# Kernel optimization log

Hardware: AMD Instinct MI355X
Metric: run time of the kernel (lower is better)

Reference implementation:

```python
import jax, jax.numpy as jnp
import numpy as np

ALPHA = 0.05  # steady-state adaptive alpha (current_step >= warmup_steps)
EPS = 1e-8    # torch cosine_similarity norm clamp

N = 8192
D = 512


def setup_inputs() -> dict:
    key = jax.random.key(0)
    k1, k2 = jax.random.split(key)
    old_emb = jax.random.normal(k1, (N, D), dtype=jnp.float32)
    new_emb = jax.random.normal(k2, (N, D), dtype=jnp.float32)
    return {"old_emb": old_emb, "new_emb": new_emb}


def _featurewise_ot(hidden_old, hidden_new, alpha):
    # nearest-neighbor match by cosine similarity (k=1 topk == argmax)
    old_n = hidden_old / jnp.maximum(jnp.linalg.norm(hidden_old, axis=1, keepdims=True), EPS)
    new_n = hidden_new / jnp.maximum(jnp.linalg.norm(hidden_new, axis=1, keepdims=True), EPS)
    sim = old_n @ new_n.T                      # [n1, n2]
    idx = jnp.argmax(sim, axis=1)              # [n1]
    expanded = hidden_new[idx]                 # [n1, d]

    # batched per-column sort-based OT alignment (replaces the python loop over d)
    h_src = jnp.sort(hidden_old, axis=0)                       # sorted old, per column
    order = jnp.argsort(expanded, axis=0)                      # idx_tgt per column
    h_tgt = jnp.take_along_axis(expanded, order, axis=0)       # sorted target, per column
    delta = alpha * (h_src - h_tgt)                            # [n1, d]
    cols = jnp.broadcast_to(jnp.arange(expanded.shape[1]), order.shape)
    update = jnp.zeros_like(expanded).at[order, cols].set(delta)  # inverse-permutation scatter
    return expanded + update


def reference(old_emb, new_emb):
    aligned_old = _featurewise_ot(old_emb, new_emb, ALPHA)
    return (1.0 - ALPHA) * new_emb + ALPHA * aligned_old
```

## Files before the change

kernel.cpp:

```cpp
#include <hip/hip_runtime.h>
#include <hip/hip_bf16.h>
#include <stdint.h>

#define NROWS 8192
#define DIM 512
#define MARGIN 0.03f
#define OVF_CAP 32

typedef unsigned long long u64;
typedef uint32_t u32;
using bf16x8 = __attribute__((ext_vector_type(8))) short;
using ushort8 = __attribute__((ext_vector_type(8))) unsigned short;
using f32x4 = __attribute__((ext_vector_type(4))) float;

__device__ __forceinline__ u32 f2o(float f){
  u32 u = __float_as_uint(f);
  return (u & 0x80000000u) ? ~u : (u | 0x80000000u);
}
__device__ __forceinline__ float o2f(u32 o){
  u32 u = (o & 0x80000000u) ? (o & 0x7FFFFFFFu) : ~o;
  return __uint_as_float(u);
}
__device__ __forceinline__ unsigned short bfbits(float f){
  __hip_bfloat16 h = __float2bfloat16(f);
  return *reinterpret_cast<unsigned short*>(&h);
}
__device__ __forceinline__ unsigned short f2o16(unsigned short b){
  return (b & 0x8000u) ? (unsigned short)~b : (unsigned short)(b | 0x8000u);
}
__device__ __forceinline__ float b16f(unsigned short b){
  u32 u = (u32)b << 16;
  return __uint_as_float(u);
}
typedef __attribute__((address_space(1))) const void gvoid;
typedef __attribute__((address_space(3))) void svoid;
__device__ __forceinline__ void gll16(const void* g, void* l){
  __builtin_amdgcn_global_load_lds((gvoid*)g, (svoid*)l, 16, 0, 0);
}

__device__ __forceinline__ int HIDX(int b){ return b + (b >> 5); }

__global__ void kconvnorm(const float* __restrict__ olde, const float* __restrict__ newe,
                          unsigned short* __restrict__ abf, unsigned short* __restrict__ bbf,
                          float* __restrict__ invn, u32* __restrict__ cnt){
  int row = blockIdx.x * 4 + (threadIdx.x >> 6);
  int lane = threadIdx.x & 63;
  if (blockIdx.x < 32) cnt[blockIdx.x * 256 + threadIdx.x] = 0u;
  bool isnew = row >= NROWS;
  int r = isnew ? row - NROWS : row;
  const float* src = (isnew ? newe : olde) + (size_t)r * DIM + lane * 8;
  unsigned short* dst = (isnew ? bbf : abf) + (size_t)r * DIM + lane * 8;
  float4 v0 = *(const float4*)src, v1 = *(const float4*)(src + 4);
  ushort8 wv = { bfbits(v0.x), bfbits(v0.y), bfbits(v0.z), bfbits(v0.w),
                 bfbits(v1.x), bfbits(v1.y), bfbits(v1.z), bfbits(v1.w) };
  *(ushort8*)dst = wv;
  if (isnew){
    float s = v0.x*v0.x + v0.y*v0.y + v0.z*v0.z + v0.w*v0.w
            + v1.x*v1.x + v1.y*v1.y + v1.z*v1.z + v1.w*v1.w;
    #pragma unroll
    for (int off = 32; off > 0; off >>= 1) s += __shfl_down(s, off);
    if (lane == 0) invn[r] = 1.0f / fmaxf(sqrtf(s), 1e-8f);
  }
}

__global__ void knorm(const float* __restrict__ x, float* __restrict__ invn,
                      u32* __restrict__ cnt){
  int row = blockIdx.x * 4 + (threadIdx.x >> 6);
  int lane = threadIdx.x & 63;
  if (threadIdx.x < 4) cnt[blockIdx.x * 4 + threadIdx.x] = 0u;
  const float4* xr = (const float4*)(x + (size_t)row * DIM);
  float s = 0.f;
  #pragma unroll
  for (int k = 0; k < 2; ++k){
    float4 v = xr[lane + 64 * k];
    s += v.x * v.x + v.y * v.y + v.z * v.z + v.w * v.w;
  }
  #pragma unroll
  for (int off = 32; off > 0; off >>= 1) s += __shfl_down(s, off);
  if (lane == 0) invn[row] = 1.0f / fmaxf(sqrtf(s), 1e-8f);
}

__device__ __forceinline__ void argmax_epilogue(
    f32x4 (&acc)[2][8], const float* __restrict__ invn,
    int m0, int n0w, int ntile, int wr, int c16, int g,
    u64* __restrict__ Tt, u64* __restrict__ ovf, u32* __restrict__ cnt){
  float invc[8];
  #pragma unroll
  for (int nj = 0; nj < 8; ++nj) invc[nj] = invn[n0w + nj * 16 + c16];
  #pragma unroll
  for (int mi = 0; mi < 2; ++mi){
    #pragma unroll
    for (int reg = 0; reg < 4; ++reg){
      float bv = -3.4e38f; int bj = 0;
      #pragma unroll
      for (int nj = 0; nj < 8; ++nj){
        float v = acc[mi][nj][reg] * invc[nj];
        if (v > bv){ bv = v; bj = nj; }
      }
      int gj = n0w + bj * 16 + c16;
      u64 pk = ((u64)f2o(bv) << 32) | (u32)(~(u32)gj);
      #pragma unroll
      for (int m = 1; m < 16; m <<= 1){
        u64 o = __shfl_xor(pk, m);
        pk = pk > o ? pk : o;
      }
      int grow = m0 + wr * 32 + mi * 16 + g * 4 + reg;
      if (c16 == 0) Tt[(size_t)grow * 64 + ntile] = pk;
      float thr = o2f((u32)(pk >> 32)) - MARGIN;
      int tj = (int)~((u32)pk);
      #pragma unroll
      for (int nj = 0; nj < 8; ++nj){
        float v = acc[mi][nj][reg] * invc[nj];
        int j = n0w + nj * 16 + c16;
        if (v >= thr && j != tj){
          u32 pos = atomicAdd(&cnt[grow], 1u);
          if (pos < OVF_CAP) ovf[(size_t)grow * OVF_CAP + pos] = ((u64)f2o(v) << 32) | (u32)j;
        }
      }
    }
  }
}

__global__ __launch_bounds__(512) void kgemm2(
    const unsigned short* __restrict__ Abf, const unsigned short* __restrict__ Bbf,
    const float* __restrict__ invn, u64* __restrict__ Tt,
    u64* __restrict__ ovf, u32* __restrict__ cnt){
  __shared__ unsigned short As[2][128 * 32];
  __shared__ unsigned short Bs[2][256 * 32];
  const int t = threadIdx.x;
  const int lane = t & 63, w = t >> 6;
  const int c16 = lane & 15, g = lane >> 4;
  const int wr = w >> 1, wc = w & 1;
  int bid = blockIdx.x;
  int xcd = bid & 7, s = bid >> 3;
  int bm = (xcd & 1) * 32 + (s >> 3);
  int bn = (xcd >> 1) * 8 + (s & 7);
  const int m0 = bm * 128, n0 = bn * 256;

  f32x4 acc[2][8];
  #pragma unroll
  for (int mi = 0; mi < 2; ++mi)
    #pragma unroll
    for (int nj = 0; nj < 8; ++nj) acc[mi][nj] = {0.f, 0.f, 0.f, 0.f};

  const int srow = t >> 2;
  const int part = t & 3;
  const int scq = (part ^ ((srow >> 1) & 3)) * 8;
  const int scq2 = (part ^ (((srow + 128) >> 1) & 3)) * 8;

  auto stage = [&](int b, int k0){
    gll16(Abf + (size_t)(m0 + srow) * DIM + k0 + scq, (void*)&As[b][(w * 16) * 32]);
    gll16(Bbf + (size_t)(n0 + srow) * DIM + k0 + scq, (void*)&Bs[b][(w * 16) * 32]);
    gll16(Bbf + (size_t)(n0 + srow + 128) * DIM + k0 + scq2, (void*)&Bs[b][(128 + w * 16) * 32]);
  };

  auto compute = [&](int b){
    bf16x8 af[2], bfr[8];
    #pragma unroll
    for (int mi = 0; mi < 2; ++mi){
      int ra = wr * 32 + mi * 16 + c16;
      af[mi] = *(const bf16x8*)&As[b][ra * 32 + (g ^ ((ra >> 1) & 3)) * 8];
    }
    #pragma unroll
    for (int nj = 0; nj < 8; ++nj){
      int rb = wc * 128 + nj * 16 + c16;
      bfr[nj] = *(const bf16x8*)&Bs[b][rb * 32 + (g ^ ((rb >> 1) & 3)) * 8];
    }
    #pragma unroll
    for (int mi = 0; mi < 2; ++mi)
      #pragma unroll
      for (int nj = 0; nj < 8; ++nj)
        acc[mi][nj] = __builtin_amdgcn_mfma_f32_16x16x32_bf16(af[mi], bfr[nj], acc[mi][nj], 0, 0, 0);
  };

  stage(0, 0);
  stage(1, 32);
  #pragma unroll 1
  for (int kt = 0; kt < 15; ++kt){
    asm volatile("s_waitcnt vmcnt(3)" ::: "memory");
    __builtin_amdgcn_s_barrier();
    compute(kt & 1);
    __builtin_amdgcn_s_barrier();
    if (kt < 14) stage(kt & 1, (kt + 2) * 32);
  }
  asm volatile("s_waitcnt vmcnt(0)" ::: "memory");
  __builtin_amdgcn_s_barrier();
  compute(1);

  argmax_epilogue(acc, invn, m0, n0 + wc * 128, bn * 2 + wc, wr, c16, g, Tt, ovf, cnt);
}

__global__ __launch_bounds__(256) void kgemm_fb(
    const float* __restrict__ A, const float* __restrict__ B,
    const float* __restrict__ invn, u64* __restrict__ Tt,
    u64* __restrict__ ovf, u32* __restrict__ cnt){
  __shared__ short As[128 * 40];
  __shared__ short Bs[128 * 40];
  const int t = threadIdx.x;
  const int lane = t & 63, w = t >> 6;
  const int c16 = lane & 15, g = lane >> 4;
  const int m0 = blockIdx.y * 128, n0 = blockIdx.x * 128;

  f32x4 acc[2][8];
  #pragma unroll
  for (int mi = 0; mi < 2; ++mi)
    #pragma unroll
    for (int nj = 0; nj < 8; ++nj) acc[mi][nj] = {0.f, 0.f, 0.f, 0.f};

  for (int k0 = 0; k0 < DIM; k0 += 32){
    #pragma unroll
    for (int it = 0; it < 2; ++it){
      int s = t + it * 256;
      int row = s >> 2, part = s & 3;
      const float4* ga = (const float4*)(A + (size_t)(m0 + row) * DIM + k0 + part * 8);
      float4 a0 = ga[0], a1 = ga[1];
      bf16x8 ha = { (short)bfbits(a0.x), (short)bfbits(a0.y), (short)bfbits(a0.z), (short)bfbits(a0.w),
                    (short)bfbits(a1.x), (short)bfbits(a1.y), (short)bfbits(a1.z), (short)bfbits(a1.w) };
      *(bf16x8*)(&As[row * 40 + part * 8]) = ha;
      const float4* gb = (const float4*)(B + (size_t)(n0 + row) * DIM + k0 + part * 8);
      float4 b0 = gb[0], b1 = gb[1];
      bf16x8 hb = { (short)bfbits(b0.x), (short)bfbits(b0.y), (short)bfbits(b0.z), (short)bfbits(b0.w),
                    (short)bfbits(b1.x), (short)bfbits(b1.y), (short)bfbits(b1.z), (short)bfbits(b1.w) };
      *(bf16x8*)(&Bs[row * 40 + part * 8]) = hb;
    }
    __syncthreads();
    bf16x8 af[2], bfr[8];
    #pragma unroll
    for (int mi = 0; mi < 2; ++mi)
      af[mi] = *(const bf16x8*)(&As[(w * 32 + mi * 16 + c16) * 40 + g * 8]);
    #pragma unroll
    for (int nj = 0; nj < 8; ++nj)
      bfr[nj] = *(const bf16x8*)(&Bs[(nj * 16 + c16) * 40 + g * 8]);
    #pragma unroll
    for (int mi = 0; mi < 2; ++mi)
      #pragma unroll
      for (int nj = 0; nj < 8; ++nj)
        acc[mi][nj] = __builtin_amdgcn_mfma_f32_16x16x32_bf16(af[mi], bfr[nj], acc[mi][nj], 0, 0, 0);
    __syncthreads();
  }
  argmax_epilogue(acc, invn, m0, n0, blockIdx.x, w, c16, g, Tt, ovf, cnt);
}

__global__ __launch_bounds__(256) void kresolve(
    const float* __restrict__ A, const float* __restrict__ B,
    const float* __restrict__ invn, const u64* __restrict__ Tt,
    const u64* __restrict__ ovf, const u32* __restrict__ cnt,
    int* __restrict__ idx){
  const int r = blockIdx.x * 4 + (threadIdx.x >> 6);
  const int lane = threadIdx.x & 63;
  u64 e = Tt[(size_t)r * 64 + lane];
  u64 m = e;
  #pragma unroll
  for (int s = 1; s < 64; s <<= 1){ u64 o = __shfl_xor(m, s); m = m > o ? m : o; }
  float W = o2f((u32)(m >> 32)) - MARGIN;
  bool inw = o2f((u32)(e >> 32)) >= W;
  u64 bal = __ballot(inw);
  u32 nov_raw = cnt[r];
  int nov = nov_raw > OVF_CAP ? OVF_CAP : (int)nov_raw;
  u64 oe = (lane < nov) ? ovf[(size_t)r * OVF_CAP + lane] : 0ull;
  bool oin = (lane < nov) && (o2f((u32)(oe >> 32)) >= W);
  u64 bal2 = __ballot(oin);
  if (nov_raw <= OVF_CAP && __popcll(bal) == 1 && bal2 == 0ull){
    if (lane == 0) idx[r] = (int)~((u32)m);
    return;
  }
  const float* ar = A + (size_t)r * DIM;
  u64 best = 0ull;
  auto eval = [&](int j){
    const float* br = B + (size_t)j * DIM;
    float s = 0.f;
    for (int k = lane; k < DIM; k += 64) s = fmaf(ar[k], br[k], s);
    #pragma unroll
    for (int o = 32; o > 0; o >>= 1) s += __shfl_xor(s, o);
    s *= invn[j];
    u64 p = ((u64)f2o(s) << 32) | (u32)(~(u32)j);
    best = best > p ? best : p;
  };
  if (nov_raw > OVF_CAP){
    for (int j = 0; j < NROWS; ++j) eval(j);
  } else {
    u64 mm = bal;
    while (mm){
      int b = __ffsll((unsigned long long)mm) - 1;
      int j = (int)~((u32)__shfl(e, b));
      eval(j);
      mm &= mm - 1;
    }
    mm = bal2;
    while (mm){
      int b = __ffsll((unsigned long long)mm) - 1;
      int j = (int)(u32)__shfl(oe, b);
      eval(j);
      mm &= mm - 1;
    }
  }
  if (lane == 0) idx[r] = (int)~((u32)best);
}

__global__ void kexpand(const float* __restrict__ newe, const int* __restrict__ idx,
                        float* __restrict__ expd){
  int i = blockIdx.x * 2 + (threadIdx.x >> 7);
  int c = (threadIdx.x & 127) * 4;
  int j = idx[i];
  *(float4*)(expd + (size_t)i * DIM + c) =
      *(const float4*)(newe + (size_t)j * DIM + c);
}

__global__ __launch_bounds__(256) void ktrans(
    const float* __restrict__ olde, unsigned short* __restrict__ oldT){
  __shared__ unsigned short tile[64][80];
  const int e0 = (blockIdx.x >> 3) * 64;
  const int c0 = (blockIdx.x & 7) * 64;
  const int t = threadIdx.x;
  {
    int r = t >> 2, cp = t & 3;
    const float4* src = (const float4*)(olde + (size_t)(e0 + r) * DIM + c0 + cp * 16);
    #pragma unroll
    for (int q = 0; q < 4; ++q){
      float4 v = src[q];
      int cc = cp * 16 + q * 4;
      tile[cc + 0][r] = bfbits(v.x);
      tile[cc + 1][r] = bfbits(v.y);
      tile[cc + 2][r] = bfbits(v.z);
      tile[cc + 3][r] = bfbits(v.w);
    }
  }
  __syncthreads();
  {
    int cR = t >> 2, ep = t & 3;
    ushort8* dst = (ushort8*)(oldT + (size_t)(c0 + cR) * NROWS + e0 + ep * 16);
    dst[0] = *(ushort8*)&tile[cR][ep * 16];
    dst[1] = *(ushort8*)&tile[cR][ep * 16 + 8];
  }
}

__device__ __forceinline__ void scan8192(u32* hist, u32* wsums, int t, int lane, int w){
  u32 v[8]; u32 ts = 0;
  #pragma unroll
  for (int k = 0; k < 8; ++k){ v[k] = hist[HIDX(t * 8 + k)]; ts += v[k]; }
  u32 inc = ts;
  #pragma unroll
  for (int off = 1; off < 64; off <<= 1){
    u32 o = (u32)__shfl_up((int)inc, off);
    if (lane >= off) inc += o;
  }
  if (lane == 63) wsums[w] = inc;
  __syncthreads();
  u32 wb = 0;
  #pragma unroll
  for (int i = 0; i < 16; ++i){ u32 x = wsums[i]; if (i < w) wb += x; }
  u32 run = wb + inc - ts;
  #pragma unroll
  for (int k = 0; k < 8; ++k){ u32 x = v[k]; hist[HIDX(t * 8 + k)] = run; run += x; }
}

__global__ __launch_bounds__(1024) void ksort4(
    const unsigned short* __restrict__ oldT, const float* __restrict__ newe,
    const int* __restrict__ idx, float* __restrict__ out){
  __shared__ u32 hist[8448];
  __shared__ unsigned short vals[NROWS];
  __shared__ u32 wsums[16];
  const int bid = blockIdx.x;
  const int c = (bid & 7) * 64 + (bid >> 3);
  const int t = threadIdx.x;
  const int lane = t & 63, w = t >> 6;

  #pragma unroll
  for (int k = 0; k < 8; ++k) hist[t + k * 1024] = 0;
  if (t < 256) hist[8192 + t] = 0;
  ushort8 ov = *(const ushort8*)(oldT + (size_t)c * NROWS + t * 8);
  __syncthreads();
  int oc[8];
  #pragma unroll
  for (int k = 0; k < 8; ++k){
    oc[k] = (int)((u32)f2o16((unsigned short)ov[k]) >> 3);
    atomicAdd(&hist[HIDX(oc[k])], 1u);
  }
  __syncthreads();
  scan8192(hist, wsums, t, lane, w);
  __syncthreads();
  #pragma unroll
  for (int k = 0; k < 8; ++k){
    u32 pos = atomicAdd(&hist[HIDX(oc[k])], 1u);
    vals[pos] = (unsigned short)ov[k];
  }
  __syncthreads();

  #pragma unroll
  for (int k = 0; k < 8; ++k) hist[t + k * 1024] = 0;
  if (t < 256) hist[8192 + t] = 0;
  __syncthreads();
  float ev[8]; int ec[8];
  #pragma unroll
  for (int k = 0; k < 8; ++k){
    int e = t + k * 1024;
    int j = idx[e];
    float x = newe[(size_t)j * DIM + c];
    ev[k] = x;
    ec[k] = (int)((u32)f2o16(bfbits(x)) >> 3);
    atomicAdd(&hist[HIDX(ec[k])], 1u);
  }
  __syncthreads();
  scan8192(hist, wsums, t, lane, w);
  __syncthreads();
  #pragma unroll
  for (int k = 0; k < 8; ++k){
    int e = t + k * 1024;
    u32 pos = atomicAdd(&hist[HIDX(ec[k])], 1u);
    float hsrc = b16f(vals[pos]);
    float aligned = fmaf(0.95f, ev[k], 0.05f * hsrc);
    out[(size_t)e * DIM + c] = fmaf(0.95f, newe[(size_t)e * DIM + c], 0.05f * aligned);
  }
}

template<bool HASPAY>
__device__ __forceinline__ void radix_pass_fb(
    u32* srcK, u32* srcP, u32* dstK, u32* dstP,
    u32* hist, u32* totals, u32* digitbase,
    int shift, int w, int lane, int t){
  for (int i = t; i < 4096; i += 1024) hist[i] = 0;
  __syncthreads();
  u32 kreg[8], preg[8], dloc[8];
  #pragma unroll
  for (int k = 0; k < 8; ++k){
    int e = w * 512 + k * 64 + lane;
    u32 key = srcK[e];
    if (HASPAY) preg[k] = srcP[e];
    kreg[k] = key;
    u32 d = (key >> shift) & 255u;
    u64 m = ~0ull;
    #pragma unroll
    for (int b = 0; b < 8; ++b){
      u64 bb = __ballot((d >> b) & 1u);
      m &= ((d >> b) & 1u) ? bb : ~bb;
    }
    int leader = __ffsll((unsigned long long)m) - 1;
    u32 rank = (u32)__popcll(m & ((1ull << lane) - 1ull));
    u32 cntg = (u32)__popcll(m);
    u32 old = 0;
    if (lane == leader){ old = hist[w * 256 + d]; hist[w * 256 + d] = old + cntg; }
    old = (u32)__shfl((int)old, leader);
    dloc[k] = (d << 16) | (old + rank);
  }
  __syncthreads();
  if (t < 256){
    u32 run = 0;
    #pragma unroll
    for (int ww = 0; ww < 16; ++ww){
      u32 v = hist[ww * 256 + t];
      hist[ww * 256 + t] = run;
      run += v;
    }
    totals[t] = run;
  }
  __syncthreads();
  if (t < 64){
    u32 carry = 0;
    #pragma unroll
    for (int ch = 0; ch < 4; ++ch){
      u32 v = totals[ch * 64 + t];
      u32 inc = v;
      #pragma unroll
      for (int off = 1; off < 64; off <<= 1){
        u32 o = (u32)__shfl_up((int)inc, off);
        if (t >= off) inc += o;
      }
      digitbase[ch * 64 + t] = carry + inc - v;
      carry += (u32)__shfl((int)inc, 63);
    }
  }
  __syncthreads();
  #pragma unroll
  for (int k = 0; k < 8; ++k){
    u32 d = dloc[k] >> 16, off = dloc[k] & 0xFFFFu;
    u32 dst = digitbase[d] + hist[w * 256 + d] + off;
    dstK[dst] = kreg[k];
    if (HASPAY) dstP[dst] = preg[k];
  }
  __syncthreads();
}

__global__ __launch_bounds__(1024) void ksort_fb(
    const float* __restrict__ olde, float* expd_out){
  __shared__ u32 buf0[NROWS], buf1[NROWS], pay0[NROWS], pay1[NROWS];
  __shared__ u32 hist[4096], totals[256], digitbase[256];
  const int bid = blockIdx.x;
  const int c = (bid & 7) * 64 + (bid >> 3);
  const int t = threadIdx.x;
  const int lane = t & 63, w = t >> 6;

  for (int e = t; e < NROWS; e += 1024){
    buf0[e] = f2o(expd_out[(size_t)e * DIM + c]);
    pay0[e] = (u32)e;
  }
  __syncthreads();
  radix_pass_fb<true>(buf0, pay0, buf1, pay1, hist, totals, digitbase, 0,  w, lane, t);
  radix_pass_fb<true>(buf1, pay1, buf0, pay0, hist, totals, digitbase, 8,  w, lane, t);
  radix_pass_fb<true>(buf0, pay0, buf1, pay1, hist, totals, digitbase, 16, w, lane, t);
  radix_pass_fb<true>(buf1, pay1, buf0, pay0, hist, totals, digitbase, 24, w, lane, t);
  for (int e = t; e < NROWS; e += 1024)
    buf1[e] = f2o(olde[(size_t)e * DIM + c]);
  __syncthreads();
  radix_pass_fb<false>(buf1, pay1, pay1, buf1, hist, totals, digitbase, 0,  w, lane, t);
  radix_pass_fb<false>(pay1, buf1, buf1, pay1, hist, totals, digitbase, 8,  w, lane, t);
  radix_pass_fb<false>(buf1, pay1, pay1, buf1, hist, totals, digitbase, 16, w, lane, t);
  radix_pass_fb<false>(pay1, buf1, buf1, pay1, hist, totals, digitbase, 24, w, lane, t);
  for (int e = t; e < NROWS; e += 1024){
    u32 row = pay0[e];
    float expv = o2f(buf0[e]);
    float hsrc = o2f(buf1[e]);
    float aligned = expv + 0.05f * (hsrc - expv);
    pay1[row] = __float_as_uint(0.05f * aligned);
  }
  __syncthreads();
  for (int e = t; e < NROWS; e += 1024)
    expd_out[(size_t)e * DIM + c] = __uint_as_float(pay1[e]);
}

__global__ void kfinal(const float* __restrict__ newe, float* __restrict__ out){
  size_t i = (size_t)blockIdx.x * 256 + threadIdx.x;
  float4 n4 = ((const float4*)newe)[i];
  float4 o4 = ((float4*)out)[i];
  o4.x = fmaf(0.95f, n4.x, o4.x);
  o4.y = fmaf(0.95f, n4.y, o4.y);
  o4.z = fmaf(0.95f, n4.z, o4.z);
  o4.w = fmaf(0.95f, n4.w, o4.w);
  ((float4*)out)[i] = o4;
}

extern "C" void kernel_launch(void* const* d_in, const int* in_sizes, int n_in,
                              void* d_out, int out_size, void* d_ws, size_t ws_size,
                              hipStream_t stream){
  const float* olde = (const float*)d_in[0];
  const float* newe = (const float*)d_in[1];
  float* out = (float*)d_out;
  int* idx = (int*)d_ws;
  float* invn = (float*)((char*)d_ws + 32768);

  const size_t WS_NEED = 65536 + (size_t)512 * NROWS * 2 + 65536;

  if (ws_size >= WS_NEED){
    unsigned short* Abf = (unsigned short*)d_out;
    unsigned short* Bbf = Abf + (size_t)NROWS * DIM;
    char* base = (char*)d_ws + 65536;
    u64* Tt  = (u64*)base;
    u64* ovf = (u64*)(base + (size_t)NROWS * 64 * 8);
    u32* cnt = (u32*)(base + (size_t)NROWS * 64 * 8 + (size_t)NROWS * OVF_CAP * 8);
    unsigned short* oldT = (unsigned short*)base;

    kconvnorm<<<2 * NROWS / 4, 256, 0, stream>>>(olde, newe, Abf, Bbf, invn, cnt);
    kgemm2<<<2048, 512, 0, stream>>>(Abf, Bbf, invn, Tt, ovf, cnt);
    kresolve<<<NROWS / 4, 256, 0, stream>>>(olde, newe, invn, Tt, ovf, cnt, idx);
    ktrans<<<1024, 256, 0, stream>>>(olde, oldT);
    ksort4<<<DIM, 1024, 0, stream>>>(oldT, newe, idx, out);
  } else {
    u64* Tt  = (u64*)d_out;
    u64* ovf = (u64*)((char*)d_out + (size_t)NROWS * 64 * 8);
    u32* cnt = (u32*)((char*)d_out + (size_t)NROWS * 64 * 8 + (size_t)NROWS * OVF_CAP * 8);

    knorm<<<NROWS / 4, 256, 0, stream>>>(newe, invn, cnt);
    kgemm_fb<<<dim3(64, 64), 256, 0, stream>>>(olde, newe, invn, Tt, ovf, cnt);
    kresolve<<<NROWS / 4, 256, 0, stream>>>(olde, newe, invn, Tt, ovf, cnt, idx);
    kexpand<<<NROWS / 2, 256, 0, stream>>>(newe, idx, out);
    ksort_fb<<<DIM, 1024, 0, stream>>>(olde, out);
    kfinal<<<NROWS * DIM / 4 / 256, 256, 0, stream>>>(newe, out);
  }
}
```

Before: 183.7 us.

## Transpose bf16 new embeddings so the column sort gathers from shared memory

Adds a kernel that transposes both bf16-converted matrices to column-major. A new column-sort kernel loads the whole new-embedding column into LDS, gathers the matched (expanded) values via idx from LDS, and writes the final blended output directly. This replaces strided fp32 global gathers from new_emb with one contiguous column load. In exchange it needs a second transposed buffer in the workspace and uses bf16-rounded new_emb values in the output blend, which lowers accuracy.

```diff
diff --git a/kernel.cpp b/kernel.cpp
--- a/kernel.cpp
+++ b/kernel.cpp
@@ -334,6 +334,34 @@
   }
 }
 
+__global__ __launch_bounds__(256) void ktrans16(
+    const unsigned short* __restrict__ srcA, const unsigned short* __restrict__ srcB,
+    unsigned short* __restrict__ dstA, unsigned short* __restrict__ dstB){
+  __shared__ unsigned short tile[64][80];
+  const bool second = blockIdx.x >= 1024;
+  const unsigned short* src = second ? srcB : srcA;
+  unsigned short* dst = second ? dstB : dstA;
+  const int b = blockIdx.x & 1023;
+  const int e0 = (b >> 3) * 64;
+  const int c0 = (b & 7) * 64;
+  const int t = threadIdx.x;
+  #pragma unroll
+  for (int p = 0; p < 2; ++p){
+    int r = (t >> 3) + p * 32;
+    int cp = t & 7;
+    ushort8 v = *(const ushort8*)(src + (size_t)(e0 + r) * DIM + c0 + cp * 8);
+    #pragma unroll
+    for (int q = 0; q < 8; ++q) tile[cp * 8 + q][r] = (unsigned short)v[q];
+  }
+  __syncthreads();
+  {
+    int cR = t >> 2, ep = t & 3;
+    ushort8* d = (ushort8*)(dst + (size_t)(c0 + cR) * NROWS + e0 + ep * 16);
+    d[0] = *(ushort8*)&tile[cR][ep * 16];
+    d[1] = *(ushort8*)&tile[cR][ep * 16 + 8];
+  }
+}
+
 __device__ __forceinline__ void scan8192(u32* hist, u32* wsums, int t, int lane, int w){
   u32 v[8]; u32 ts = 0;
   #pragma unroll
@@ -352,6 +380,70 @@
   u32 run = wb + inc - ts;
   #pragma unroll
   for (int k = 0; k < 8; ++k){ u32 x = v[k]; hist[HIDX(t * 8 + k)] = run; run += x; }
+}
+
+__global__ __launch_bounds__(1024) void ksort5(
+    const unsigned short* __restrict__ oldT, const unsigned short* __restrict__ newT,
+    const int* __restrict__ idx, float* __restrict__ out){
+  __shared__ u32 hist[8448];
+  __shared__ unsigned short vals[NROWS];
+  __shared__ unsigned short ncol[NROWS];
+  __shared__ u32 wsums[16];
+  const int bid = blockIdx.x;
+  const int c = (bid & 7) * 64 + (bid >> 3);
+  const int t = threadIdx.x;
+  const int lane = t & 63, w = t >> 6;
+
+  *(ushort8*)&ncol[t * 8] = *(const ushort8*)(newT + (size_t)c * NROWS + t * 8);
+  #pragma unroll
+  for (int k = 0; k < 8; ++k) hist[t + k * 1024] = 0;
+  if (t < 256) hist[8192 + t] = 0;
+  ushort8 ov = *(const ushort8*)(oldT + (size_t)c * NROWS + t * 8);
+  __syncthreads();
+
+  int oc[8];
+  #pragma unroll
+  for (int k = 0; k < 8; ++k){
+    oc[k] = (int)((u32)f2o16((unsigned short)ov[k]) >> 3);
+    atomicAdd(&hist[HIDX(oc[k])], 1u);
+  }
+  __syncthreads();
+  scan8192(hist, wsums, t, lane, w);
+  __syncthreads();
+  #pragma unroll
+  for (int k = 0; k < 8; ++k){
+    u32 pos = atomicAdd(&hist[HIDX(oc[k])], 1u);
+    vals[pos] = (unsigned short)ov[k];
+  }
+  __syncthreads();
+
+  #pragma unroll
+  for (int k = 0; k < 8; ++k) hist[t + k * 1024] = 0;
+  if (t < 256) hist[8192 + t] = 0;
+  int j_[8];
+  #pragma unroll
+  for (int k = 0; k < 8; ++k) j_[k] = idx[t + k * 1024];
+  __syncthreads();
+  unsigned short evc[8]; int ec[8];
+  #pragma unroll
+  for (int k = 0; k < 8; ++k){
+    evc[k] = ncol[j_[k]];
+    ec[k] = (int)((u32)f2o16(evc[k]) >> 3);
+    atomicAdd(&hist[HIDX(ec[k])], 1u);
+  }
+  __syncthreads();
+  scan8192(hist, wsums, t, lane, w);
+  __syncthreads();
+  #pragma unroll
+  for (int k = 0; k < 8; ++k){
+    int e = t + k * 1024;
+    u32 pos = atomicAdd(&hist[HIDX(ec[k])], 1u);
+    float hsrc = b16f(vals[pos]);
+    float ev = b16f(evc[k]);
+    float nv = b16f(ncol[e]);
+    float aligned = fmaf(0.95f, ev, 0.05f * hsrc);
+    out[(size_t)e * DIM + c] = fmaf(0.95f, nv, 0.05f * aligned);
+  }
 }
 
 __global__ __launch_bounds__(1024) void ksort4(
@@ -537,9 +629,11 @@
   int* idx = (int*)d_ws;
   float* invn = (float*)((char*)d_ws + 32768);
 
-  const size_t WS_NEED = 65536 + (size_t)512 * NROWS * 2 + 65536;
-
-  if (ws_size >= WS_NEED){
+  const size_t MATB = (size_t)NROWS * DIM * 2;
+  const size_t WS_T1 = 65536 + 2 * MATB + 65536;
+  const size_t WS_T2 = 65536 + MATB + 65536;
+
+  if (ws_size >= WS_T2){
     unsigned short* Abf = (unsigned short*)d_out;
     unsigned short* Bbf = Abf + (size_t)NROWS * DIM;
     char* base = (char*)d_ws + 65536;
@@ -547,12 +641,18 @@
     u64* ovf = (u64*)(base + (size_t)NROWS * 64 * 8);
     u32* cnt = (u32*)(base + (size_t)NROWS * 64 * 8 + (size_t)NROWS * OVF_CAP * 8);
     unsigned short* oldT = (unsigned short*)base;
+    unsigned short* newT = (unsigned short*)(base + MATB);
 
     kconvnorm<<<2 * NROWS / 4, 256, 0, stream>>>(olde, newe, Abf, Bbf, invn, cnt);
     kgemm2<<<2048, 512, 0, stream>>>(Abf, Bbf, invn, Tt, ovf, cnt);
     kresolve<<<NROWS / 4, 256, 0, stream>>>(olde, newe, invn, Tt, ovf, cnt, idx);
-    ktrans<<<1024, 256, 0, stream>>>(olde, oldT);
-    ksort4<<<DIM, 1024, 0, stream>>>(oldT, newe, idx, out);
+    if (ws_size >= WS_T1){
+      ktrans16<<<2048, 256, 0, stream>>>(Abf, Bbf, oldT, newT);
+      ksort5<<<DIM, 1024, 0, stream>>>(oldT, newT, idx, out);
+    } else {
+      ktrans<<<1024, 256, 0, stream>>>(olde, oldT);
+      ksort4<<<DIM, 1024, 0, stream>>>(oldT, newe, idx, out);
+    }
   } else {
     u64* Tt  = (u64*)d_out;
     u64* ovf = (u64*)((char*)d_out + (size_t)NROWS * 64 * 8);
```

Result: faster. 164.9 us, median of 3 (-10.2%).
